# Kernel optimization log

Hardware: AMD Instinct MI355X
Metric: run time of the kernel (lower is better)

## Reference

```python
import jax, jax.numpy as jnp
import numpy as np

BATCH = 2048
FID_NUM = 65536
AVG_ACTIVE = 20.0  # ~active fids per example


def setup_inputs() -> dict:
    key = jax.random.key(0)
    k1, k2, k3 = jax.random.split(key, 3)
    # binary one-hot gate, ~AVG_ACTIVE ones per row (matches _get_model_feed_dict)
    gate = (jax.random.uniform(k1, (BATCH, FID_NUM)) < (AVG_ACTIVE / FID_NUM)).astype(jnp.float32)
    sparse_bias = 0.01 * jax.random.normal(k2, (FID_NUM,), dtype=jnp.float32)
    global_bias = jnp.zeros((1,), dtype=jnp.float32)
    label = (jax.random.uniform(k3, (BATCH,)) < 0.5).astype(jnp.float32)
    return {"bias_fid_gate": gate, "sparse_bias": sparse_bias,
            "global_bias": global_bias, "label": label}


def reference(bias_fid_gate, sparse_bias, global_bias, label):
    # bias_input = gate * bias; logits = reduce_sum(bias_input, axis=1) + global_bias
    logits = jnp.sum(bias_fid_gate * sparse_bias, axis=1) + global_bias[0]  # [B]
    pred = jax.nn.sigmoid(logits)
    # tf.nn.sigmoid_cross_entropy_with_logits, then reduce_sum
    per_ex = jnp.maximum(logits, 0.0) - logits * label + jnp.log1p(jnp.exp(-jnp.abs(logits)))
    loss = jnp.sum(per_ex)
    return logits, pred, loss
```

## Files before the change

### kernel.cpp

```cpp
#include <hip/hip_runtime.h>
#include <math.h>

#define BATCH 2048
#define FID 65536
#define NT 256
#define NV (FID / 4)

typedef float vf4 __attribute__((ext_vector_type(4)));

__global__ __launch_bounds__(NT, 8) void lr_row(
        const float* __restrict__ gate,
        const float* __restrict__ bias,
        float* __restrict__ out) {
    const int r = blockIdx.x;
    const vf4* __restrict__ b4 = (const vf4*)bias;
    const vf4* __restrict__ g4 = (const vf4*)gate + (size_t)r * NV;

    float a = 0.f;
    #pragma unroll 4
    for (int i = threadIdx.x; i < NV; i += NT) {
        vf4 v = b4[i];
        vf4 g = __builtin_nontemporal_load(&g4[i]);
        a = fmaf(g.x, v.x, a);
        a = fmaf(g.y, v.y, a);
        a = fmaf(g.z, v.z, a);
        a = fmaf(g.w, v.w, a);
    }

    #pragma unroll
    for (int off = 32; off > 0; off >>= 1)
        a += __shfl_down(a, off, 64);

    __shared__ float wsum[NT / 64];
    const int wave = threadIdx.x >> 6;
    const int lane = threadIdx.x & 63;
    if (lane == 0) wsum[wave] = a;
    __syncthreads();
    if (threadIdx.x == 0)
        out[r] = wsum[0] + wsum[1] + wsum[2] + wsum[3];
}

__global__ __launch_bounds__(NT) void lr_finish(
        const float* __restrict__ gbias,
        const float* __restrict__ label,
        float* __restrict__ out) {
    const float gb = gbias[0];
    float acc = 0.0f;
    for (int i = threadIdx.x; i < BATCH; i += NT) {
        float x = out[i] + gb;
        float l = label[i];
        out[i] = x;
        out[BATCH + i] = 1.0f / (1.0f + expf(-x));
        acc += fmaxf(x, 0.0f) - x * l + log1pf(expf(-fabsf(x)));
    }
    #pragma unroll
    for (int off = 32; off > 0; off >>= 1)
        acc += __shfl_down(acc, off, 64);

    __shared__ float wsum[NT / 64];
    const int wave = threadIdx.x >> 6;
    const int lane = threadIdx.x & 63;
    if (lane == 0) wsum[wave] = acc;
    __syncthreads();
    if (threadIdx.x == 0)
        out[2 * BATCH] = wsum[0] + wsum[1] + wsum[2] + wsum[3];
}

extern "C" void kernel_launch(void* const* d_in, const int* in_sizes, int n_in,
                              void* d_out, int out_size, void* d_ws, size_t ws_size,
                              hipStream_t stream) {
    const float* gate  = (const float*)d_in[0];
    const float* bias  = (const float*)d_in[1];
    const float* gbias = (const float*)d_in[2];
    const float* label = (const float*)d_in[3];
    float* out = (float*)d_out;

    lr_row<<<BATCH, NT, 0, stream>>>(gate, bias, out);
    lr_finish<<<1, NT, 0, stream>>>(gbias, label, out);
}
```

Baseline: 654.5 us.

## Sweep gate in column chunks with register-resident bias and per-wave partial sums

Each block now owns one 1024-vf4 column chunk of the feature dimension, keeps its slice of sparse_bias in registers, and strides over rows, so bias is no longer reloaded for every row. Each wave reduces its 256 columns and writes a partial sum to a workspace slot. The finish kernel then adds the 64 partials per row before the sigmoid and loss. This cuts redundant bias traffic and the per-block LDS sync, at the cost of a per-iteration wave shuffle reduction, scattered small workspace writes, and a heavier single-block finish pass.

```diff
diff --git a/kernel.cpp b/kernel.cpp
--- a/kernel.cpp
+++ b/kernel.cpp
@@ -5,52 +5,80 @@
 #define FID 65536
 #define NT 256
 #define NV (FID / 4)
+#define GRID 2048
+#define CHUNK 1024
+#define CPR (NV / CHUNK)
+#define NIT (BATCH * NV / (GRID * CHUNK))
+#define SLOTS 64
 
 typedef float vf4 __attribute__((ext_vector_type(4)));
 
-__global__ __launch_bounds__(NT, 8) void lr_row(
+__global__ __launch_bounds__(NT, 8) void lr_sweep(
         const float* __restrict__ gate,
         const float* __restrict__ bias,
-        float* __restrict__ out) {
-    const int r = blockIdx.x;
+        float* __restrict__ ws) {
+    const int bid  = blockIdx.x;
+    const int tid  = threadIdx.x;
+    const int wave = tid >> 6;
+    const int lane = tid & 63;
     const vf4* __restrict__ b4 = (const vf4*)bias;
-    const vf4* __restrict__ g4 = (const vf4*)gate + (size_t)r * NV;
+    const vf4* __restrict__ g4 = (const vf4*)gate;
 
-    float a = 0.f;
-    #pragma unroll 4
-    for (int i = threadIdx.x; i < NV; i += NT) {
-        vf4 v = b4[i];
-        vf4 g = __builtin_nontemporal_load(&g4[i]);
-        a = fmaf(g.x, v.x, a);
-        a = fmaf(g.y, v.y, a);
-        a = fmaf(g.z, v.z, a);
-        a = fmaf(g.w, v.w, a);
+    const int bb = (bid & (CPR - 1)) * CHUNK + tid;
+    const vf4 v0 = b4[bb];
+    const vf4 v1 = b4[bb + NT];
+    const vf4 v2 = b4[bb + 2 * NT];
+    const vf4 v3 = b4[bb + 3 * NT];
+
+    const vf4* __restrict__ gp = g4 + (size_t)bid * CHUNK + tid;
+    const int slot = (bid & (CPR - 1)) * 4 + wave;
+    const int row0 = bid >> 4;
+
+    for (int t = 0; t < NIT; ++t) {
+        const vf4* p = gp + (size_t)t * (GRID * CHUNK);
+        vf4 g0 = __builtin_nontemporal_load(&p[0]);
+        vf4 g1 = __builtin_nontemporal_load(&p[NT]);
+        vf4 g2 = __builtin_nontemporal_load(&p[2 * NT]);
+        vf4 g3 = __builtin_nontemporal_load(&p[3 * NT]);
+
+        float a = g0.x * v0.x;
+        a = fmaf(g0.y, v0.y, a); a = fmaf(g0.z, v0.z, a); a = fmaf(g0.w, v0.w, a);
+        a = fmaf(g1.x, v1.x, a); a = fmaf(g1.y, v1.y, a);
+        a = fmaf(g1.z, v1.z, a); a = fmaf(g1.w, v1.w, a);
+        float b = g2.x * v2.x;
+        b = fmaf(g2.y, v2.y, b); b = fmaf(g2.z, v2.z, b); b = fmaf(g2.w, v2.w, b);
+        b = fmaf(g3.x, v3.x, b); b = fmaf(g3.y, v3.y, b);
+        b = fmaf(g3.z, v3.z, b); b = fmaf(g3.w, v3.w, b);
+        a += b;
+
+        #pragma unroll
+        for (int off = 32; off > 0; off >>= 1)
+            a += __shfl_down(a, off, 64);
+
+        if (lane == 0)
+            ws[(size_t)(row0 + t * (GRID / CPR)) * SLOTS + slot] = a;
     }
-
-    #pragma unroll
-    for (int off = 32; off > 0; off >>= 1)
-        a += __shfl_down(a, off, 64);
-
-    __shared__ float wsum[NT / 64];
-    const int wave = threadIdx.x >> 6;
-    const int lane = threadIdx.x & 63;
-    if (lane == 0) wsum[wave] = a;
-    __syncthreads();
-    if (threadIdx.x == 0)
-        out[r] = wsum[0] + wsum[1] + wsum[2] + wsum[3];
 }
 
 __global__ __launch_bounds__(NT) void lr_finish(
+        const float* __restrict__ ws,
         const float* __restrict__ gbias,
         const float* __restrict__ label,
         float* __restrict__ out) {
     const float gb = gbias[0];
     float acc = 0.0f;
-    for (int i = threadIdx.x; i < BATCH; i += NT) {
-        float x = out[i] + gb;
-        float l = label[i];
-        out[i] = x;
-        out[BATCH + i] = 1.0f / (1.0f + expf(-x));
+    for (int r = threadIdx.x; r < BATCH; r += NT) {
+        const vf4* w = (const vf4*)(ws + (size_t)r * SLOTS);
+        vf4 s4 = w[0];
+        #pragma unroll
+        for (int j = 1; j < SLOTS / 4; ++j) {
+            vf4 t = w[j];
+            s4.x += t.x; s4.y += t.y; s4.z += t.z; s4.w += t.w;
+        }
+        float x = (s4.x + s4.y) + (s4.z + s4.w) + gb;
+        float l = label[r];
+        out[r] = x;
+        out[BATCH + r] = 1.0f / (1.0f + expf(-x));
         acc += fmaxf(x, 0.0f) - x * l + log1pf(expf(-fabsf(x)));
     }
     #pragma unroll
@@ -74,7 +102,8 @@
     const float* gbias = (const float*)d_in[2];
     const float* label = (const float*)d_in[3];
     float* out = (float*)d_out;
+    float* ws  = (float*)d_ws;
 
-    lr_row<<<BATCH, NT, 0, stream>>>(gate, bias, out);
-    lr_finish<<<1, NT, 0, stream>>>(gbias, label, out);
+    lr_sweep<<<GRID, NT, 0, stream>>>(gate, bias, ws);
+    lr_finish<<<1, NT, 0, stream>>>(ws, gbias, label, out);
 }
```

New measurement: 664.2 us (median of 2 runs). About the same (+1.5%).
